# Kernel tuning notes

Measured on AMD Instinct MI355X. Metric: run time of the kernel, lower is better.

The kernel has to match this reference:

```python
import jax, jax.numpy as jnp
import numpy as np

N = 50000        # nodes
E = 800000       # edges (avg degree 16)
NFEAT = 16       # 14 feat + 2 pos
NHID = 64
NCLASS = 1
NGRAPHS = 500
NLAYERS = 5
DT, ALPHA, GAMMA = 1.0, 1.0, 1.0


def _lin_init(k, fan_in, fan_out):
    # torch nn.Linear default: U(-1/sqrt(fan_in), 1/sqrt(fan_in))
    lim = 1.0 / np.sqrt(fan_in)
    kw, kb = jax.random.split(k)
    W = jax.random.uniform(kw, (fan_in, fan_out), minval=-lim, maxval=lim, dtype=jnp.float32)
    b = jax.random.uniform(kb, (fan_out,), minval=-lim, maxval=lim, dtype=jnp.float32)
    return W, b


def setup_inputs() -> dict:
    key = jax.random.key(0)
    ks = jax.random.split(key, 8)
    x = jax.random.normal(ks[0], (N, 14), dtype=jnp.float32)
    pos = jax.random.normal(ks[1], (N, 2), dtype=jnp.float32)
    edge_index = jax.random.randint(ks[2], (2, E), 0, N, dtype=jnp.int64)
    batch = jnp.sort(jax.random.randint(ks[3], (N,), 0, NGRAPHS, dtype=jnp.int64))
    enc_W, enc_b = _lin_init(ks[4], NFEAT, NHID)
    conv_W, conv_b = _lin_init(ks[5], NHID, NHID)
    res_W, res_b = _lin_init(ks[6], NHID, NHID)
    dec_W, dec_b = _lin_init(ks[7], NHID, NCLASS)
    return dict(x=x, pos=pos, edge_index=edge_index, batch=batch,
                enc_W=enc_W, enc_b=enc_b, conv_W=conv_W, conv_b=conv_b,
                res_W=res_W, res_b=res_b, dec_W=dec_W, dec_b=dec_b)


def _gcn_conv(h, src, dst, W, b):
    # PyG GCNConv: add self-loops, symmetric normalization, scatter-add to dst.
    loop = jnp.arange(N, dtype=src.dtype)
    src2 = jnp.concatenate([src, loop])
    dst2 = jnp.concatenate([dst, loop])
    deg = jax.ops.segment_sum(jnp.ones_like(dst2, dtype=h.dtype), dst2, num_segments=N)
    dinv = jnp.where(deg > 0, jax.lax.rsqrt(deg), 0.0)
    hW = h @ W                                   # [N, nhid]
    norm = dinv[src2] * dinv[dst2]               # [E+N]
    msg = hW[src2] * norm[:, None]               # [E+N, nhid]
    return jax.ops.segment_sum(msg, dst2, num_segments=N) + b


def reference(x, pos, edge_index, batch, enc_W, enc_b, conv_W, conv_b, res_W, res_b, dec_W, dec_b):
    src, dst = edge_index[0], edge_index[1]
    inp = jnp.concatenate([x, pos], axis=-1)     # [N, nfeat]
    Y = inp @ enc_W + enc_b
    X = Y
    # dropout p=0 -> identity (eval mode)
    for _ in range(NLAYERS):
        agg = _gcn_conv(X, src, dst, conv_W, conv_b) + (X @ res_W + res_b)
        Y = Y + DT * (jax.nn.relu(agg) - ALPHA * Y - GAMMA * X)
        X = X + DT * Y
    Xo = X @ dec_W + dec_b                       # [N, 1]
    pooled = jax.ops.segment_sum(Xo, batch, num_segments=NGRAPHS)  # [G, 1]
    return pooled.squeeze(-1)                    # [G]
```

## Files before the change

### kernel.cpp

```cpp
#include <hip/hip_runtime.h>

#define NN 50000
#define NE 800000
#define NH 64
#define NG 500
#define NPAD 50176
#define NBKT 782
#define CAP 1536
#define ZR NN

typedef __attribute__((ext_vector_type(8))) short bf16x8;
typedef __attribute__((ext_vector_type(4))) float f32x4;

__device__ __forceinline__ unsigned short f2bf(float f) {
  unsigned x = __float_as_uint(f);
  unsigned r = ((x >> 16) & 1u) + 0x7fffu;
  return (unsigned short)((x + r) >> 16);
}
__device__ __forceinline__ float bf2f(unsigned short u) {
  return __uint_as_float(((unsigned)u) << 16);
}


__global__ __launch_bounds__(256) void k_prep(const float* __restrict__ Wc, const float* __restrict__ Wr,
                                              unsigned short* __restrict__ Wf,
                                              int* __restrict__ bcur,
                                              unsigned short* __restrict__ hWbf) {
  if (blockIdx.x == 8) {
    int tt = threadIdx.x;
    for (int i = tt; i < 1024; i += 256) bcur[i] = 0;
    if (tt < 32) ((unsigned*)(hWbf + (size_t)ZR * 64))[tt] = 0u;
    return;
  }
  int t = blockIdx.x * 256 + threadIdx.x;
  int fid = t >> 6;
  int lane = t & 63;
  int ntile = fid & 3, s = (fid >> 2) & 1, part = (fid >> 3) & 1, mat = fid >> 4;
  const float* W = mat ? Wr : Wc;
  int col = ntile * 16 + (lane & 15);
  int k0 = s * 32 + (lane >> 4) * 8;
#pragma unroll
  for (int e = 0; e < 8; e++) {
    float w = W[(k0 + e) * 64 + col];
    unsigned short h = f2bf(w);
    Wf[(size_t)fid * 512 + lane * 8 + e] = part ? f2bf(w - bf2f(h)) : h;
  }
}


__global__ __launch_bounds__(256) void k_bin(const int* __restrict__ src, const int* __restrict__ dst,
                                             int* __restrict__ bcur, int* __restrict__ colp) {
  __shared__ int hist[NBKT];
  __shared__ int gbase[NBKT];
  int t = threadIdx.x;
  for (int b = t; b < NBKT; b += 256) hist[b] = 0;
  __syncthreads();
  int e0 = blockIdx.x * 8192;
#pragma unroll
  for (int i = 0; i < 32; i++) {
    int e = e0 + i * 256 + t;
    if (e < NE) atomicAdd(&hist[dst[e] >> 6], 1);
  }
  __syncthreads();
  for (int b = t; b < NBKT; b += 256) {
    int c = hist[b];
    gbase[b] = c ? atomicAdd(&bcur[b], c) : 0;
    hist[b] = 0;
  }
  __syncthreads();
#pragma unroll
  for (int i = 0; i < 32; i++) {
    int e = e0 + i * 256 + t;
    if (e < NE) {
      int s = src[e], d = dst[e];
      int b = d >> 6;
      int r = atomicAdd(&hist[b], 1);
      colp[b * CAP + gbase[b] + r] = (s << 6) | (d & 63);
    }
  }
}


template <int MODE>
__device__ __forceinline__ void gemm_tile(int lane, int n0,
                                          const float* __restrict__ Xin,
                                          const unsigned short* __restrict__ gsum,
                                          const unsigned short* __restrict__ Wf,
                                          const float* __restrict__ cb, const float* __restrict__ rb,
                                          const float* __restrict__ dinv,
                                          unsigned short* __restrict__ hWout, float* __restrict__ agg) {
  int col16 = lane & 15;
  int kb = lane >> 4;
  int nr = n0 + col16;
  int nc = nr < NN ? nr : NN - 1;
  const float* xrow = Xin + (size_t)nc * 64;
  float v0[8], v1[8];
  {
    float4 a = *(const float4*)(xrow + kb * 8);
    float4 b4 = *(const float4*)(xrow + kb * 8 + 4);
    float4 c = *(const float4*)(xrow + 32 + kb * 8);
    float4 d = *(const float4*)(xrow + 32 + kb * 8 + 4);
    v0[0] = a.x; v0[1] = a.y; v0[2] = a.z; v0[3] = a.w;
    v0[4] = b4.x; v0[5] = b4.y; v0[6] = b4.z; v0[7] = b4.w;
    v1[0] = c.x; v1[1] = c.y; v1[2] = c.z; v1[3] = c.w;
    v1[4] = d.x; v1[5] = d.y; v1[6] = d.z; v1[7] = d.w;
  }
  if (MODE) {
    float dvn = dinv[nc];
    const unsigned* grow = (const unsigned*)(gsum + (size_t)nc * 64);
    uint4 g0 = *(const uint4*)(grow + kb * 4);
    uint4 g1 = *(const uint4*)(grow + 16 + kb * 4);
    unsigned ga[4] = {g0.x, g0.y, g0.z, g0.w};
    unsigned gb[4] = {g1.x, g1.y, g1.z, g1.w};
#pragma unroll
    for (int e = 0; e < 4; e++) {
      v0[2 * e]     = fmaxf(v0[2 * e]     + dvn * bf2f((unsigned short)(ga[e] & 0xffff)), 0.f);
      v0[2 * e + 1] = fmaxf(v0[2 * e + 1] + dvn * bf2f((unsigned short)(ga[e] >> 16)), 0.f);
      v1[2 * e]     = fmaxf(v1[2 * e]     + dvn * bf2f((unsigned short)(gb[e] & 0xffff)), 0.f);
      v1[2 * e + 1] = fmaxf(v1[2 * e + 1] + dvn * bf2f((unsigned short)(gb[e] >> 16)), 0.f);
    }
  }
  bf16x8 ah0, al0, ah1, al1;
#pragma unroll
  for (int e = 0; e < 8; e++) {
    unsigned short h0 = f2bf(v0[e]);
    ah0[e] = (short)h0;
    al0[e] = (short)f2bf(v0[e] - bf2f(h0));
    unsigned short h1 = f2bf(v1[e]);
    ah1[e] = (short)h1;
    al1[e] = (short)f2bf(v1[e] - bf2f(h1));
  }

  f32x4 aC[4], aR[4];
#pragma unroll
  for (int j = 0; j < 4; j++) {
    aC[j] = (f32x4){0.f, 0.f, 0.f, 0.f};
    aR[j] = (f32x4){0.f, 0.f, 0.f, 0.f};
  }
  const bf16x8* WFv = (const bf16x8*)Wf;
#pragma unroll
  for (int j = 0; j < 4; j++) {
    bf16x8 wch0 = WFv[(j)      * 64 + lane];
    bf16x8 wch1 = WFv[(4 + j)  * 64 + lane];
    bf16x8 wcl0 = WFv[(8 + j)  * 64 + lane];
    bf16x8 wcl1 = WFv[(12 + j) * 64 + lane];
    bf16x8 wrh0 = WFv[(16 + j) * 64 + lane];
    bf16x8 wrh1 = WFv[(20 + j) * 64 + lane];
    bf16x8 wrl0 = WFv[(24 + j) * 64 + lane];
    bf16x8 wrl1 = WFv[(28 + j) * 64 + lane];
    f32x4 c = aC[j];
    c = __builtin_amdgcn_mfma_f32_16x16x32_bf16(ah0, wch0, c, 0, 0, 0);
    c = __builtin_amdgcn_mfma_f32_16x16x32_bf16(ah1, wch1, c, 0, 0, 0);
    c = __builtin_amdgcn_mfma_f32_16x16x32_bf16(al0, wch0, c, 0, 0, 0);
    c = __builtin_amdgcn_mfma_f32_16x16x32_bf16(al1, wch1, c, 0, 0, 0);
    c = __builtin_amdgcn_mfma_f32_16x16x32_bf16(ah0, wcl0, c, 0, 0, 0);
    c = __builtin_amdgcn_mfma_f32_16x16x32_bf16(ah1, wcl1, c, 0, 0, 0);
    aC[j] = c;
    f32x4 r = aR[j];
    r = __builtin_amdgcn_mfma_f32_16x16x32_bf16(ah0, wrh0, r, 0, 0, 0);
    r = __builtin_amdgcn_mfma_f32_16x16x32_bf16(ah1, wrh1, r, 0, 0, 0);
    r = __builtin_amdgcn_mfma_f32_16x16x32_bf16(al0, wrh0, r, 0, 0, 0);
    r = __builtin_amdgcn_mfma_f32_16x16x32_bf16(al1, wrh1, r, 0, 0, 0);
    r = __builtin_amdgcn_mfma_f32_16x16x32_bf16(ah0, wrl0, r, 0, 0, 0);
    r = __builtin_amdgcn_mfma_f32_16x16x32_bf16(ah1, wrl1, r, 0, 0, 0);
    aR[j] = r;
  }

  float cbv[4], rbv[4];
#pragma unroll
  for (int j = 0; j < 4; j++) {
    cbv[j] = cb[j * 16 + col16];
    rbv[j] = rb[j * 16 + col16];
  }
  int rbase = kb * 4;
#pragma unroll
  for (int r = 0; r < 4; r++) {
    int node = n0 + rbase + r;
    if (node < NN) {
      float dv = dinv[node];
      size_t o = (size_t)node * 64 + col16;
#pragma unroll
      for (int j = 0; j < 4; j++) {
        float hc = dv * aC[j][r];
        unsigned short hb = f2bf(hc);
        hWout[o + j * 16] = hb;
        agg[o + j * 16] = aR[j][r] + rbv[j] + cbv[j] + dv * hc;
      }
    }
  }
}


__global__ __launch_bounds__(256) void k_csr_enc_g0(const int* __restrict__ bcur, const int* __restrict__ colp,
                                                    int* __restrict__ cols, float* __restrict__ dinv,
                                                    int2* __restrict__ rows2,
                                                    const int* __restrict__ batch, int* __restrict__ gptr,
                                                    const float* __restrict__ x, const float* __restrict__ pos,
                                                    const float* __restrict__ encW, const float* __restrict__ encb,
                                                    const unsigned short* __restrict__ Wf,
                                                    const float* __restrict__ cb, const float* __restrict__ rb,
                                                    unsigned short* __restrict__ hWout,
                                                    float* __restrict__ X0, float* __restrict__ agg) {
  __shared__ int hist[64];
  __shared__ int excl[65];
  __shared__ float Ws[16 * 64];
  __shared__ float bs[64];
  int t = threadIdx.x;
  int b = blockIdx.x;

  int tid = b * 256 + t;
  if (tid < NN) {
    int bi = batch[tid];
    int bp = (tid > 0) ? batch[tid - 1] : -1;
    for (int g = bp + 1; g <= bi; g++) gptr[g] = tid;
    if (tid == NN - 1) {
      for (int g = bi + 1; g <= NG; g++) gptr[g] = NN;
    }
  }

  for (int i = t; i < 1024; i += 256) Ws[i] = encW[i];
  if (t < 64) bs[t] = encb[t];

  int base = b * CAP;
  int cnt = bcur[b];
  if (t < 64) hist[t] = 0;
  __syncthreads();
  for (int e = t; e < cnt; e += 256) atomicAdd(&hist[colp[base + e] & 63], 1);
  __syncthreads();
  if (t == 0) {
    int run = 0;
#pragma unroll
    for (int i = 0; i < 64; i++) { excl[i] = run; run += hist[i]; }
    excl[64] = run;
  }
  __syncthreads();
  if (t < 64) {
    int n = b * 64 + t;
    rows2[n] = make_int2(base + excl[t], base + excl[t + 1]);
    if (n < NN) dinv[n] = rsqrtf((float)(hist[t] + 1));
    hist[t] = 0;
  }
  __syncthreads();
  for (int e = t; e < cnt; e += 256) {
    int w = colp[base + e];
    int d = w & 63;
    int r = atomicAdd(&hist[d], 1);
    cols[base + excl[d] + r] = w >> 6;
  }

  int h = t & 63;
  int nset = t >> 6;
#pragma unroll
  for (int i = 0; i < 16; i++) {
    int n = b * 64 + nset * 16 + i;
    if (n < NN) {
      const float* xr = x + n * 14;
      float acc = bs[h];
#pragma unroll
      for (int f = 0; f < 14; f++) acc += xr[f] * Ws[f * 64 + h];
      acc += pos[n * 2 + 0] * Ws[14 * 64 + h];
      acc += pos[n * 2 + 1] * Ws[15 * 64 + h];
      X0[(size_t)n * 64 + h] = acc;
    }
  }
  __syncthreads();

  gemm_tile<0>(t & 63, b * 64 + (t >> 6) * 16, X0, (const unsigned short*)0, Wf, cb, rb, dinv, hWout, agg);
}


__global__ __launch_bounds__(256) void k_gemm(const float* __restrict__ Xin,
                                              const unsigned short* __restrict__ gsum,
                                              const unsigned short* __restrict__ Wf,
                                              const float* __restrict__ cb, const float* __restrict__ rb,
                                              const float* __restrict__ dinv,
                                              unsigned short* __restrict__ hWout, float* __restrict__ agg) {
  gemm_tile<1>(threadIdx.x & 63, blockIdx.x * 64 + (threadIdx.x >> 6) * 16,
               Xin, gsum, Wf, cb, rb, dinv, hWout, agg);
}


__device__ __forceinline__ void gather_node(int n, int lane, int h2, int p,
                                            const int2* __restrict__ rows2,
                                            const int* __restrict__ cols, const unsigned* __restrict__ hW32,
                                            float& a0, float& a1) {
  int2 se = rows2[n];
  int st = se.x;
  int deg = se.y - se.x;
  a0 = 0.f; a1 = 0.f;
  for (int base2 = 0; base2 < deg; base2 += 64) {
    int cnt = deg - base2;
    if (cnt > 64) cnt = 64;
    int li = lane < cnt ? lane : cnt - 1;
    int colv = cols[st + base2 + li];
    for (int j = 0; j < cnt; j += 16) {
      int sx[8];
#pragma unroll
      for (int k2 = 0; k2 < 8; k2++) {
        int e = j + 2 * k2 + p;
        int s = __shfl(colv, e, 64);
        sx[k2] = e < cnt ? s : ZR;
      }
      unsigned ux[8];
#pragma unroll
      for (int k2 = 0; k2 < 8; k2++) ux[k2] = hW32[(unsigned)sx[k2] * 32u + (unsigned)h2];
#pragma unroll
      for (int k2 = 0; k2 < 8; k2++) {
        a0 += __uint_as_float(ux[k2] << 16);
        a1 += __uint_as_float(ux[k2] & 0xffff0000u);
      }
    }
  }
  a0 += __shfl_down(a0, 32, 64);
  a1 += __shfl_down(a1, 32, 64);
}


__global__ __launch_bounds__(256, 8) void k_gather(const int2* __restrict__ rows2,
                                                   const int* __restrict__ cols,
                                                   const unsigned short* __restrict__ hWin,
                                                   unsigned short* __restrict__ gsum) {
  int lane = threadIdx.x & 63;
  int h2 = lane & 31;
  int p = lane >> 5;
  int n = __builtin_amdgcn_readfirstlane(blockIdx.x * 4 + (threadIdx.x >> 6));
  float a0, a1;
  gather_node(n, lane, h2, p, rows2, cols, (const unsigned*)hWin, a0, a1);
  if (lane < 32)
    ((unsigned*)gsum)[(unsigned)n * 32u + (unsigned)h2] = (unsigned)f2bf(a0) | ((unsigned)f2bf(a1) << 16);
}


__global__ __launch_bounds__(256, 8) void k_gather_final(const int2* __restrict__ rows2,
                                                         const int* __restrict__ cols,
                                                         const unsigned short* __restrict__ hWin,
                                                         const float* __restrict__ aggIn, const float* __restrict__ dinv,
                                                         const float* __restrict__ decW, float* __restrict__ Xo) {
  int lane = threadIdx.x & 63;
  int h2 = lane & 31;
  int p = lane >> 5;
  int n = __builtin_amdgcn_readfirstlane(blockIdx.x * 4 + (threadIdx.x >> 6));
  float a0, a1;
  gather_node(n, lane, h2, p, rows2, cols, (const unsigned*)hWin, a0, a1);
  float dv = dinv[n];
  float2 ag = *(const float2*)(aggIn + (size_t)n * 64 + h2 * 2);
  float v = fmaxf(ag.x + dv * a0, 0.f) * decW[h2 * 2] + fmaxf(ag.y + dv * a1, 0.f) * decW[h2 * 2 + 1];
  v = (lane < 32) ? v : 0.f;
#pragma unroll
  for (int off = 32; off > 0; off >>= 1) v += __shfl_down(v, off, 64);
  if (lane == 0) Xo[n] = v;
}


__global__ __launch_bounds__(256) void k_pool(const float* __restrict__ Xo, const int* __restrict__ gptr,
                                              const float* __restrict__ decb, float* __restrict__ out) {
  __shared__ float part[4];
  int g = blockIdx.x;
  int t = threadIdx.x;
  int st = gptr[g], en = gptr[g + 1];
  float v = 0.f;
  for (int i = st + t; i < en; i += 256) v += Xo[i];
#pragma unroll
  for (int off = 32; off > 0; off >>= 1) v += __shfl_down(v, off, 64);
  if ((t & 63) == 0) part[t >> 6] = v;
  __syncthreads();
  if (t == 0) out[g] = part[0] + part[1] + part[2] + part[3] + (float)(en - st) * decb[0];
}


extern "C" void kernel_launch(void* const* d_in, const int* in_sizes, int n_in,
                              void* d_out, int out_size, void* d_ws, size_t ws_size,
                              hipStream_t stream) {
  (void)in_sizes; (void)n_in; (void)out_size; (void)ws_size;
  const float* x     = (const float*)d_in[0];
  const float* pos   = (const float*)d_in[1];
  const int*   ei    = (const int*)d_in[2];
  const int*   batch = (const int*)d_in[3];
  const float* encW  = (const float*)d_in[4];
  const float* encb  = (const float*)d_in[5];
  const float* convW = (const float*)d_in[6];
  const float* convb = (const float*)d_in[7];
  const float* resW  = (const float*)d_in[8];
  const float* resb  = (const float*)d_in[9];
  const float* decW  = (const float*)d_in[10];
  const float* decb  = (const float*)d_in[11];
  float* out = (float*)d_out;

  const int* src = ei;
  const int* dst = ei + NE;

  float*          ws    = (float*)d_ws;
  float*          dinv  = ws;
  int2*           rows2 = (int2*)(ws + NPAD);
  int*            bcur  = (int*)(ws + 3 * NPAD);
  int*            gptr  = bcur + 1024;
  float*          Xo    = (float*)(gptr + 512);
  int*            colp  = (int*)(Xo + NPAD);
  int*            cols  = colp + NBKT * CAP;
  unsigned short* hWbf  = (unsigned short*)(cols + NBKT * CAP);
  unsigned short* gsum  = hWbf + (size_t)NPAD * 64;
  float*          bufA  = (float*)(gsum + (size_t)NPAD * 64);
  float*          bufB  = bufA + NN * NH;
  unsigned short* Wf    = (unsigned short*)(bufB + NN * NH);

  k_prep<<<9, 256, 0, stream>>>(convW, resW, Wf, bcur, hWbf);
  k_bin<<<(NE + 8191) / 8192, 256, 0, stream>>>(src, dst, bcur, colp);
  k_csr_enc_g0<<<NBKT, 256, 0, stream>>>(bcur, colp, cols, dinv, rows2, batch, gptr,
                                         x, pos, encW, encb, Wf, convb, resb,
                                         hWbf, bufA, bufB);
  float* aggIn = bufB;
  float* aggOut = bufA;
  for (int l = 0; l < 4; l++) {
    k_gather<<<NN / 4, 256, 0, stream>>>(rows2, cols, hWbf, gsum);
    k_gemm<<<NBKT, 256, 0, stream>>>(aggIn, gsum, Wf, convb, resb, dinv, hWbf, aggOut);
    float* tmp = aggIn; aggIn = aggOut; aggOut = tmp;
  }
  k_gather_final<<<NN / 4, 256, 0, stream>>>(rows2, cols, hWbf, aggIn, dinv, decW, Xo);
  k_pool<<<NG, 256, 0, stream>>>(Xo, gptr, decb, out);
}
```

Measured before the change: 274.2 us.

## Split bf16 hidden features into two column halves for cache-friendlier gathers

Stores the bf16 hW matrix as two separate planes of 32 columns each (64 bytes per node row) and launches the gather kernels twice as wide, with each block half working on one plane. Each gathered row now fills one 64-byte line instead of 128 bytes, and each plane is half the size, which should give a better L2 hit rate for the random neighbour reads. In exchange the CSR column indices are read twice, there are twice as many wavefronts, and the final decoder reduction writes two partial outputs that the pool kernel adds together.

```diff
diff --git a/kernel.cpp b/kernel.cpp
--- a/kernel.cpp
+++ b/kernel.cpp
@@ -8,6 +8,7 @@
 #define NBKT 782
 #define CAP 1536
 #define ZR NN
+#define NBH 12500
 
 typedef __attribute__((ext_vector_type(8))) short bf16x8;
 typedef __attribute__((ext_vector_type(4))) float f32x4;
@@ -29,7 +30,10 @@
   if (blockIdx.x == 8) {
     int tt = threadIdx.x;
     for (int i = tt; i < 1024; i += 256) bcur[i] = 0;
-    if (tt < 32) ((unsigned*)(hWbf + (size_t)ZR * 64))[tt] = 0u;
+    if (tt < 16) {
+      ((unsigned*)hWbf)[((size_t)(0 * NPAD + ZR)) * 16 + tt] = 0u;
+      ((unsigned*)hWbf)[((size_t)(1 * NPAD + ZR)) * 16 + tt] = 0u;
+    }
     return;
   }
   int t = blockIdx.x * 256 + threadIdx.x;
@@ -183,7 +187,7 @@
       for (int j = 0; j < 4; j++) {
         float hc = dv * aC[j][r];
         unsigned short hb = f2bf(hc);
-        hWout[o + j * 16] = hb;
+        hWout[((size_t)((j >> 1) * NPAD + node)) * 32 + (j & 1) * 16 + col16] = hb;
         agg[o + j * 16] = aR[j][r] + rbv[j] + cbv[j] + dv * hc;
       }
     }
@@ -280,9 +284,9 @@
 }
 
 
-__device__ __forceinline__ void gather_node(int n, int lane, int h2, int p,
+__device__ __forceinline__ void gather_half(int n, int lane, int w, int q,
                                             const int2* __restrict__ rows2,
-                                            const int* __restrict__ cols, const unsigned* __restrict__ hW32,
+                                            const int* __restrict__ cols, const unsigned* __restrict__ hw,
                                             float& a0, float& a1) {
   int2 se = rows2[n];
   int st = se.x;
@@ -293,17 +297,17 @@
     if (cnt > 64) cnt = 64;
     int li = lane < cnt ? lane : cnt - 1;
     int colv = cols[st + base2 + li];
-    for (int j = 0; j < cnt; j += 16) {
+    for (int j = 0; j < cnt; j += 32) {
       int sx[8];
 #pragma unroll
       for (int k2 = 0; k2 < 8; k2++) {
-        int e = j + 2 * k2 + p;
+        int e = j + 4 * k2 + q;
         int s = __shfl(colv, e, 64);
         sx[k2] = e < cnt ? s : ZR;
       }
       unsigned ux[8];
 #pragma unroll
-      for (int k2 = 0; k2 < 8; k2++) ux[k2] = hW32[(unsigned)sx[k2] * 32u + (unsigned)h2];
+      for (int k2 = 0; k2 < 8; k2++) ux[k2] = hw[(unsigned)sx[k2] * 16u + (unsigned)w];
 #pragma unroll
       for (int k2 = 0; k2 < 8; k2++) {
         a0 += __uint_as_float(ux[k2] << 16);
@@ -313,6 +317,8 @@
   }
   a0 += __shfl_down(a0, 32, 64);
   a1 += __shfl_down(a1, 32, 64);
+  a0 += __shfl_down(a0, 16, 64);
+  a1 += __shfl_down(a1, 16, 64);
 }
 
 
@@ -320,14 +326,18 @@
                                                    const int* __restrict__ cols,
                                                    const unsigned short* __restrict__ hWin,
                                                    unsigned short* __restrict__ gsum) {
-  int lane = threadIdx.x & 63;
-  int h2 = lane & 31;
-  int p = lane >> 5;
-  int n = __builtin_amdgcn_readfirstlane(blockIdx.x * 4 + (threadIdx.x >> 6));
+  int t = threadIdx.x;
+  int lane = t & 63;
+  int w = lane & 15;
+  int q = lane >> 4;
+  int half = blockIdx.x >= NBH ? 1 : 0;
+  int n = __builtin_amdgcn_readfirstlane((blockIdx.x - half * NBH) * 4 + (t >> 6));
+  const unsigned* hw = (const unsigned*)hWin + (size_t)half * NPAD * 16;
   float a0, a1;
-  gather_node(n, lane, h2, p, rows2, cols, (const unsigned*)hWin, a0, a1);
-  if (lane < 32)
-    ((unsigned*)gsum)[(unsigned)n * 32u + (unsigned)h2] = (unsigned)f2bf(a0) | ((unsigned)f2bf(a1) << 16);
+  gather_half(n, lane, w, q, rows2, cols, hw, a0, a1);
+  if (lane < 16)
+    ((unsigned*)gsum)[(unsigned)n * 32u + (unsigned)(half * 16 + w)] =
+        (unsigned)f2bf(a0) | ((unsigned)f2bf(a1) << 16);
 }
 
 
@@ -335,31 +345,35 @@
                                                          const int* __restrict__ cols,
                                                          const unsigned short* __restrict__ hWin,
                                                          const float* __restrict__ aggIn, const float* __restrict__ dinv,
-                                                         const float* __restrict__ decW, float* __restrict__ Xo) {
-  int lane = threadIdx.x & 63;
-  int h2 = lane & 31;
-  int p = lane >> 5;
-  int n = __builtin_amdgcn_readfirstlane(blockIdx.x * 4 + (threadIdx.x >> 6));
+                                                         const float* __restrict__ decW, float* __restrict__ Xo2) {
+  int t = threadIdx.x;
+  int lane = t & 63;
+  int w = lane & 15;
+  int q = lane >> 4;
+  int half = blockIdx.x >= NBH ? 1 : 0;
+  int n = __builtin_amdgcn_readfirstlane((blockIdx.x - half * NBH) * 4 + (t >> 6));
+  const unsigned* hw = (const unsigned*)hWin + (size_t)half * NPAD * 16;
   float a0, a1;
-  gather_node(n, lane, h2, p, rows2, cols, (const unsigned*)hWin, a0, a1);
+  gather_half(n, lane, w, q, rows2, cols, hw, a0, a1);
   float dv = dinv[n];
-  float2 ag = *(const float2*)(aggIn + (size_t)n * 64 + h2 * 2);
-  float v = fmaxf(ag.x + dv * a0, 0.f) * decW[h2 * 2] + fmaxf(ag.y + dv * a1, 0.f) * decW[h2 * 2 + 1];
-  v = (lane < 32) ? v : 0.f;
-#pragma unroll
-  for (int off = 32; off > 0; off >>= 1) v += __shfl_down(v, off, 64);
-  if (lane == 0) Xo[n] = v;
-}
-
-
-__global__ __launch_bounds__(256) void k_pool(const float* __restrict__ Xo, const int* __restrict__ gptr,
+  int hword = half * 16 + w;
+  float2 ag = ((const float2*)aggIn)[(size_t)n * 32 + hword];
+  float v = fmaxf(ag.x + dv * a0, 0.f) * decW[hword * 2] + fmaxf(ag.y + dv * a1, 0.f) * decW[hword * 2 + 1];
+  v = (lane < 16) ? v : 0.f;
+#pragma unroll
+  for (int off = 8; off > 0; off >>= 1) v += __shfl_down(v, off, 64);
+  if (lane == 0) Xo2[(size_t)half * NPAD + n] = v;
+}
+
+
+__global__ __launch_bounds__(256) void k_pool(const float* __restrict__ Xo2, const int* __restrict__ gptr,
                                               const float* __restrict__ decb, float* __restrict__ out) {
   __shared__ float part[4];
   int g = blockIdx.x;
   int t = threadIdx.x;
   int st = gptr[g], en = gptr[g + 1];
   float v = 0.f;
-  for (int i = st + t; i < en; i += 256) v += Xo[i];
+  for (int i = st + t; i < en; i += 256) v += Xo2[i] + Xo2[NPAD + i];
 #pragma unroll
   for (int off = 32; off > 0; off >>= 1) v += __shfl_down(v, off, 64);
   if ((t & 63) == 0) part[t >> 6] = v;
@@ -394,8 +408,8 @@
   int2*           rows2 = (int2*)(ws + NPAD);
   int*            bcur  = (int*)(ws + 3 * NPAD);
   int*            gptr  = bcur + 1024;
-  float*          Xo    = (float*)(gptr + 512);
-  int*            colp  = (int*)(Xo + NPAD);
+  float*          Xo2   = (float*)(gptr + 512);
+  int*            colp  = (int*)(Xo2 + 2 * NPAD);
   int*            cols  = colp + NBKT * CAP;
   unsigned short* hWbf  = (unsigned short*)(cols + NBKT * CAP);
   unsigned short* gsum  = hWbf + (size_t)NPAD * 64;
@@ -411,10 +425,10 @@
   float* aggIn = bufB;
   float* aggOut = bufA;
   for (int l = 0; l < 4; l++) {
-    k_gather<<<NN / 4, 256, 0, stream>>>(rows2, cols, hWbf, gsum);
+    k_gather<<<2 * NBH, 256, 0, stream>>>(rows2, cols, hWbf, gsum);
     k_gemm<<<NBKT, 256, 0, stream>>>(aggIn, gsum, Wf, convb, resb, dinv, hWbf, aggOut);
     float* tmp = aggIn; aggIn = aggOut; aggOut = tmp;
   }
-  k_gather_final<<<NN / 4, 256, 0, stream>>>(rows2, cols, hWbf, aggIn, dinv, decW, Xo);
-  k_pool<<<NG, 256, 0, stream>>>(Xo, gptr, decb, out);
-}
+  k_gather_final<<<2 * NBH, 256, 0, stream>>>(rows2, cols, hWbf, aggIn, dinv, decW, Xo2);
+  k_pool<<<NG, 256, 0, stream>>>(Xo2, gptr, decb, out);
+}
```

New measurement: 314.5 us. 1.15x slower.

## Split neighbor gather into two source-range passes for cache locality

Applied to the files above, without the earlier changes.

Partitions each node's CSR neighbor list by source index (below or above a midpoint) and runs the gather in two kernel passes, each touching only half of the hW table. The aim is to make each pass's random reads fit in the L2/MALL cache. The cost is an extra kernel launch per layer and an fp32 partial-sum buffer that is written and read back.

```diff
diff --git a/kernel.cpp b/kernel.cpp
--- a/kernel.cpp
+++ b/kernel.cpp
@@ -8,6 +8,7 @@
 #define NBKT 782
 #define CAP 1536
 #define ZR NN
+#define SH 25088
 
 typedef __attribute__((ext_vector_type(8))) short bf16x8;
 typedef __attribute__((ext_vector_type(4))) float f32x4;
@@ -193,7 +194,7 @@
 
 __global__ __launch_bounds__(256) void k_csr_enc_g0(const int* __restrict__ bcur, const int* __restrict__ colp,
                                                     int* __restrict__ cols, float* __restrict__ dinv,
-                                                    int2* __restrict__ rows2,
+                                                    int2* __restrict__ rows2, int* __restrict__ midg,
                                                     const int* __restrict__ batch, int* __restrict__ gptr,
                                                     const float* __restrict__ x, const float* __restrict__ pos,
                                                     const float* __restrict__ encW, const float* __restrict__ encb,
@@ -201,8 +202,9 @@
                                                     const float* __restrict__ cb, const float* __restrict__ rb,
                                                     unsigned short* __restrict__ hWout,
                                                     float* __restrict__ X0, float* __restrict__ agg) {
-  __shared__ int hist[64];
+  __shared__ int h0c[64], h1c[64];
   __shared__ int excl[65];
+  __shared__ int midS[64];
   __shared__ float Ws[16 * 64];
   __shared__ float bs[64];
   int t = threadIdx.x;
@@ -223,29 +225,41 @@
 
   int base = b * CAP;
   int cnt = bcur[b];
-  if (t < 64) hist[t] = 0;
-  __syncthreads();
-  for (int e = t; e < cnt; e += 256) atomicAdd(&hist[colp[base + e] & 63], 1);
+  if (t < 64) { h0c[t] = 0; h1c[t] = 0; }
+  __syncthreads();
+  for (int e = t; e < cnt; e += 256) {
+    int w = colp[base + e];
+    if ((w >> 6) < SH) atomicAdd(&h0c[w & 63], 1); else atomicAdd(&h1c[w & 63], 1);
+  }
   __syncthreads();
   if (t == 0) {
     int run = 0;
 #pragma unroll
-    for (int i = 0; i < 64; i++) { excl[i] = run; run += hist[i]; }
+    for (int i = 0; i < 64; i++) { excl[i] = run; run += h0c[i] + h1c[i]; }
     excl[64] = run;
   }
   __syncthreads();
   if (t < 64) {
     int n = b * 64 + t;
     rows2[n] = make_int2(base + excl[t], base + excl[t + 1]);
-    if (n < NN) dinv[n] = rsqrtf((float)(hist[t] + 1));
-    hist[t] = 0;
-  }
+    int m = excl[t] + h0c[t];
+    midS[t] = m;
+    midg[n] = base + m;
+    if (n < NN) dinv[n] = rsqrtf((float)(h0c[t] + h1c[t] + 1));
+  }
+  __syncthreads();
+  if (t < 64) { h0c[t] = 0; h1c[t] = 0; }
   __syncthreads();
   for (int e = t; e < cnt; e += 256) {
     int w = colp[base + e];
-    int d = w & 63;
-    int r = atomicAdd(&hist[d], 1);
-    cols[base + excl[d] + r] = w >> 6;
+    int d = w & 63, s = w >> 6;
+    if (s < SH) {
+      int r = atomicAdd(&h0c[d], 1);
+      cols[base + excl[d] + r] = s;
+    } else {
+      int r = atomicAdd(&h1c[d], 1);
+      cols[base + midS[d] + r] = s;
+    }
   }
 
   int h = t & 63;
@@ -280,13 +294,10 @@
 }
 
 
-__device__ __forceinline__ void gather_node(int n, int lane, int h2, int p,
-                                            const int2* __restrict__ rows2,
-                                            const int* __restrict__ cols, const unsigned* __restrict__ hW32,
-                                            float& a0, float& a1) {
-  int2 se = rows2[n];
-  int st = se.x;
-  int deg = se.y - se.x;
+__device__ __forceinline__ void gather_seg(int st, int en, int lane, int h2, int p,
+                                           const int* __restrict__ cols, const unsigned* __restrict__ hW32,
+                                           float& a0, float& a1) {
+  int deg = en - st;
   a0 = 0.f; a1 = 0.f;
   for (int base2 = 0; base2 < deg; base2 += 64) {
     int cnt = deg - base2;
@@ -316,32 +327,59 @@
 }
 
 
-__global__ __launch_bounds__(256, 8) void k_gather(const int2* __restrict__ rows2,
-                                                   const int* __restrict__ cols,
-                                                   const unsigned short* __restrict__ hWin,
-                                                   unsigned short* __restrict__ gsum) {
+__global__ __launch_bounds__(256, 8) void k_gather_p0(const int2* __restrict__ rows2, const int* __restrict__ midg,
+                                                      const int* __restrict__ cols,
+                                                      const unsigned short* __restrict__ hWin,
+                                                      float* __restrict__ gpart) {
   int lane = threadIdx.x & 63;
   int h2 = lane & 31;
   int p = lane >> 5;
   int n = __builtin_amdgcn_readfirstlane(blockIdx.x * 4 + (threadIdx.x >> 6));
   float a0, a1;
-  gather_node(n, lane, h2, p, rows2, cols, (const unsigned*)hWin, a0, a1);
-  if (lane < 32)
-    ((unsigned*)gsum)[(unsigned)n * 32u + (unsigned)h2] = (unsigned)f2bf(a0) | ((unsigned)f2bf(a1) << 16);
-}
-
-
-__global__ __launch_bounds__(256, 8) void k_gather_final(const int2* __restrict__ rows2,
-                                                         const int* __restrict__ cols,
-                                                         const unsigned short* __restrict__ hWin,
-                                                         const float* __restrict__ aggIn, const float* __restrict__ dinv,
-                                                         const float* __restrict__ decW, float* __restrict__ Xo) {
+  gather_seg(rows2[n].x, midg[n], lane, h2, p, cols, (const unsigned*)hWin, a0, a1);
+  if (lane < 32) {
+    float* gp = gpart + ((size_t)n * 32 + h2) * 2;
+    __builtin_nontemporal_store(a0, gp);
+    __builtin_nontemporal_store(a1, gp + 1);
+  }
+}
+
+
+__global__ __launch_bounds__(256, 8) void k_gather_p1(const int2* __restrict__ rows2, const int* __restrict__ midg,
+                                                      const int* __restrict__ cols,
+                                                      const unsigned short* __restrict__ hWin,
+                                                      const float* __restrict__ gpart,
+                                                      unsigned short* __restrict__ gsum) {
   int lane = threadIdx.x & 63;
   int h2 = lane & 31;
   int p = lane >> 5;
   int n = __builtin_amdgcn_readfirstlane(blockIdx.x * 4 + (threadIdx.x >> 6));
   float a0, a1;
-  gather_node(n, lane, h2, p, rows2, cols, (const unsigned*)hWin, a0, a1);
+  gather_seg(midg[n], rows2[n].y, lane, h2, p, cols, (const unsigned*)hWin, a0, a1);
+  if (lane < 32) {
+    const float* gp = gpart + ((size_t)n * 32 + h2) * 2;
+    a0 += __builtin_nontemporal_load(gp);
+    a1 += __builtin_nontemporal_load(gp + 1);
+    ((unsigned*)gsum)[(unsigned)n * 32u + (unsigned)h2] = (unsigned)f2bf(a0) | ((unsigned)f2bf(a1) << 16);
+  }
+}
+
+
+__global__ __launch_bounds__(256, 8) void k_gather_f1(const int2* __restrict__ rows2, const int* __restrict__ midg,
+                                                      const int* __restrict__ cols,
+                                                      const unsigned short* __restrict__ hWin,
+                                                      const float* __restrict__ gpart,
+                                                      const float* __restrict__ aggIn, const float* __restrict__ dinv,
+                                                      const float* __restrict__ decW, float* __restrict__ Xo) {
+  int lane = threadIdx.x & 63;
+  int h2 = lane & 31;
+  int p = lane >> 5;
+  int n = __builtin_amdgcn_readfirstlane(blockIdx.x * 4 + (threadIdx.x >> 6));
+  float a0, a1;
+  gather_seg(midg[n], rows2[n].y, lane, h2, p, cols, (const unsigned*)hWin, a0, a1);
+  const float* gp = gpart + ((size_t)n * 32 + h2) * 2;
+  a0 += __builtin_nontemporal_load(gp);
+  a1 += __builtin_nontemporal_load(gp + 1);
   float dv = dinv[n];
   float2 ag = *(const float2*)(aggIn + (size_t)n * 64 + h2 * 2);
   float v = fmaxf(ag.x + dv * a0, 0.f) * decW[h2 * 2] + fmaxf(ag.y + dv * a1, 0.f) * decW[h2 * 2 + 1];
@@ -392,29 +430,33 @@
   float*          ws    = (float*)d_ws;
   float*          dinv  = ws;
   int2*           rows2 = (int2*)(ws + NPAD);
-  int*            bcur  = (int*)(ws + 3 * NPAD);
+  int*            midg  = (int*)(ws + 3 * NPAD);
+  int*            bcur  = (int*)(ws + 4 * NPAD);
   int*            gptr  = bcur + 1024;
   float*          Xo    = (float*)(gptr + 512);
   int*            colp  = (int*)(Xo + NPAD);
   int*            cols  = colp + NBKT * CAP;
   unsigned short* hWbf  = (unsigned short*)(cols + NBKT * CAP);
   unsigned short* gsum  = hWbf + (size_t)NPAD * 64;
-  float*          bufA  = (float*)(gsum + (size_t)NPAD * 64);
+  float*          gpart = (float*)(gsum + (size_t)NPAD * 64);
+  float*          bufA  = gpart + (size_t)NPAD * 64;
   float*          bufB  = bufA + NN * NH;
   unsigned short* Wf    = (unsigned short*)(bufB + NN * NH);
 
   k_prep<<<9, 256, 0, stream>>>(convW, resW, Wf, bcur, hWbf);
   k_bin<<<(NE + 8191) / 8192, 256, 0, stream>>>(src, dst, bcur, colp);
-  k_csr_enc_g0<<<NBKT, 256, 0, stream>>>(bcur, colp, cols, dinv, rows2, batch, gptr,
+  k_csr_enc_g0<<<NBKT, 256, 0, stream>>>(bcur, colp, cols, dinv, rows2, midg, batch, gptr,
                                          x, pos, encW, encb, Wf, convb, resb,
                                          hWbf, bufA, bufB);
   float* aggIn = bufB;
   float* aggOut = bufA;
   for (int l = 0; l < 4; l++) {
-    k_gather<<<NN / 4, 256, 0, stream>>>(rows2, cols, hWbf, gsum);
+    k_gather_p0<<<NN / 4, 256, 0, stream>>>(rows2, midg, cols, hWbf, gpart);
+    k_gather_p1<<<NN / 4, 256, 0, stream>>>(rows2, midg, cols, hWbf, gpart, gsum);
     k_gemm<<<NBKT, 256, 0, stream>>>(aggIn, gsum, Wf, convb, resb, dinv, hWbf, aggOut);
     float* tmp = aggIn; aggIn = aggOut; aggOut = tmp;
   }
-  k_gather_final<<<NN / 4, 256, 0, stream>>>(rows2, cols, hWbf, aggIn, dinv, decW, Xo);
+  k_gather_p0<<<NN / 4, 256, 0, stream>>>(rows2, midg, cols, hWbf, gpart);
+  k_gather_f1<<<NN / 4, 256, 0, stream>>>(rows2, midg, cols, hWbf, gpart, aggIn, dinv, decW, Xo);
   k_pool<<<NG, 256, 0, stream>>>(Xo, gptr, decb, out);
 }
```

Result: slower. 336.9 us (+22.8%).
